# Kernel tuning notes

Hardware: AMD Instinct MI355X
Metric: run time of the kernel (lower is better)

The kernel has to match this reference:

```python
import jax, jax.numpy as jnp
import numpy as np

L_ORDER = 1
R_ORDER = 1
THRESHOLD = 1.0


def setup_inputs() -> dict:
    key = jax.random.key(0)
    k0, k1, k2, k3, k4 = jax.random.split(key, 5)
    B, T, D, K = 16, 2048, 512, L_ORDER + R_ORDER + 1
    hidden = jax.random.normal(k0, (B, T, D), jnp.float32)
    conv_w = jax.random.normal(k1, (D, 1, K), jnp.float32) / np.sqrt(K).astype(np.float32)
    conv_b = jax.random.normal(k2, (D,), jnp.float32) * 0.05
    lin_w = jax.random.normal(k3, (1, D), jnp.float32) / np.sqrt(D).astype(np.float32)
    lin_b = jax.random.normal(k4, (1,), jnp.float32) * 0.05
    return {"hidden": hidden, "conv_w": conv_w, "conv_b": conv_b, "lin_w": lin_w, "lin_b": lin_b}


def _alphas(hidden, conv_w, conv_b, lin_w, lin_b):
    # hidden: [B, T, D]
    ctx = jnp.transpose(hidden, (0, 2, 1))              # [B, D, T]
    q = jnp.pad(ctx, ((0, 0), (0, 0), (L_ORDER, R_ORDER)))
    mem = jax.lax.conv_general_dilated(
        q, conv_w, (1,), 'VALID',
        dimension_numbers=('NCH', 'OIH', 'NCH'),
        feature_group_count=ctx.shape[1]) + conv_b[None, :, None]   # depthwise conv
    out = jax.nn.relu(jnp.transpose(mem + ctx, (0, 2, 1)))          # [B, T, D] (dropout = identity in eval)
    logits = out @ lin_w.T + lin_b                                  # [B, T, 1]
    return jax.nn.sigmoid(logits)[..., 0]                           # [B, T]


def _cif_scan(hidden, alphas):
    # Sequential integrate-and-fire recurrence over time via lax.scan.
    B, T, H = hidden.shape

    def step(carry, xs):
        integ, frame = carry        # [B], [B, H]
        a, h = xs                   # [B], [B, H]
        dist = 1.0 - integ
        integ = integ + a
        fire_out = integ            # recorded pre-reset (matches torch list_fires)
        fire = integ >= THRESHOLD
        integ = jnp.where(fire, integ - 1.0, integ)
        cur = jnp.where(fire, dist, a)
        rem = a - cur
        frame_out = frame + cur[:, None] * h   # recorded pre-reset
        frame = jnp.where(fire[:, None], rem[:, None] * h, frame_out)
        return (integ, frame), (fire_out, frame_out)

    init = (jnp.zeros((B,), hidden.dtype), jnp.zeros((B, H), hidden.dtype))
    _, (fires, frames) = jax.lax.scan(
        step, init, (alphas.T, jnp.transpose(hidden, (1, 0, 2))))
    return jnp.transpose(fires, (1, 0)), jnp.transpose(frames, (1, 0, 2))  # [B,T], [B,T,H]


def reference(hidden, conv_w, conv_b, lin_w, lin_b):
    B, T, H = hidden.shape
    alphas = _alphas(hidden, conv_w, conv_b, lin_w, lin_b)   # [B, T]
    token_num = alphas.sum(-1)                               # [B]
    fires, frames = _cif_scan(hidden, alphas)
    # Ragged extraction: gather frames at fire positions, left-packed, zero-padded
    # to max_label_len = max(round(sum alphas)). Data-dependent length -> python int.
    max_label_len = int(jnp.max(jnp.round(token_num)))
    fire_mask = fires >= THRESHOLD                           # [B, T]
    rank = jnp.cumsum(fire_mask, axis=1) - 1                 # output slot per fire
    b_idx = jnp.arange(B)[:, None]
    vals = jnp.where(fire_mask[..., None], frames, 0.0)
    acoustic_embeds = jnp.zeros((B, max_label_len, H), hidden.dtype)
    acoustic_embeds = acoustic_embeds.at[b_idx, rank].add(vals, mode='drop')
    return acoustic_embeds, token_num, alphas, fires
```

## Files before the change

### kernel.cpp

```cpp
#include <hip/hip_runtime.h>
#include <math.h>

#define B_ 16
#define T_ 2048
#define D_ 512


__global__ __launch_bounds__(256) void k_alphas(
    const float* __restrict__ hidden,
    const float* __restrict__ conv_w,
    const float* __restrict__ conv_b,
    const float* __restrict__ lin_w,
    const float* __restrict__ lin_b,
    float* __restrict__ alphas_out)
{
    const int b    = blockIdx.y;
    const int wv   = threadIdx.x >> 6;
    const int lane = threadIdx.x & 63;
    const int t0   = blockIdx.x * 64 + wv * 16;
    const int d0   = lane * 8;

    float w0[8], w1[8], w2[8], cb[8], lw[8];
    #pragma unroll
    for (int i = 0; i < 8; ++i) {
        int d = d0 + i;
        w0[i] = conv_w[3 * d];
        w1[i] = conv_w[3 * d + 1];
        w2[i] = conv_w[3 * d + 2];
        cb[i] = conv_b[d];
        lw[i] = lin_w[d];
    }
    const float lb = lin_b[0];

    const float* rbase = hidden + (size_t)b * T_ * D_ + d0;
    auto loadrow = [&](int t, float* f) {
        const float4* p = (const float4*)(rbase + (size_t)t * D_);
        float4 x = p[0], y = p[1];
        f[0]=x.x; f[1]=x.y; f[2]=x.z; f[3]=x.w;
        f[4]=y.x; f[5]=y.y; f[6]=y.z; f[7]=y.w;
    };

    float hm[8], hc[8], hp[8], nx[8];
    if (t0 > 0) { loadrow(t0 - 1, hm); }
    else        { for (int i = 0; i < 8; ++i) hm[i] = 0.f; }
    loadrow(t0, hc);
    loadrow(t0 + 1, hp);

    float* aout = alphas_out + (size_t)b * T_;
    #pragma unroll 4
    for (int j = 0; j < 16; ++j) {
        const int t = t0 + j;
        const int tn = t + 2;
        if (tn < T_) { loadrow(tn, nx); }
        else         { for (int i = 0; i < 8; ++i) nx[i] = 0.f; }

        float dot = 0.f;
        #pragma unroll
        for (int i = 0; i < 8; ++i) {
            float mem = fmaf(hm[i], w0[i],
                        fmaf(hc[i], w1[i],
                        fmaf(hp[i], w2[i], cb[i])));
            float o = mem + hc[i];
            o = o > 0.f ? o : 0.f;
            dot += o * lw[i];
        }
        #pragma unroll
        for (int off = 32; off > 0; off >>= 1) dot += __shfl_down(dot, off);
        if (lane == 0) aout[t] = 1.f / (1.f + expf(-(dot + lb)));

        #pragma unroll
        for (int i = 0; i < 8; ++i) { hm[i] = hc[i]; hc[i] = hp[i]; hp[i] = nx[i]; }
    }
}

__global__ __launch_bounds__(256) void k_scan(
    const float* __restrict__ alphas_in,
    double* __restrict__ S,
    int*    __restrict__ fire_pos,
    int*    __restrict__ n_fires,
    float*  __restrict__ fires_out,
    float*  __restrict__ token_out)
{
    const int b = blockIdx.x, tid = threadIdx.x;
    const size_t base = (size_t)b * T_;

    double a[8], tsum = 0.0;
    #pragma unroll
    for (int i = 0; i < 8; ++i) { a[i] = (double)alphas_in[base + tid * 8 + i]; tsum += a[i]; }

    __shared__ double ssum[256];
    ssum[tid] = tsum;
    __syncthreads();
    for (int off = 1; off < 256; off <<= 1) {
        double v = (tid >= off) ? ssum[tid - off] : 0.0;
        __syncthreads();
        ssum[tid] += v;
        __syncthreads();
    }
    double run = ssum[tid] - tsum;

    #pragma unroll
    for (int i = 0; i < 8; ++i) {
        int t = tid * 8 + i;
        double Sp = run, fp = floor(Sp);
        run += a[i];
        S[base + t] = run;
        fires_out[base + t] = (float)(run - fp);
        if (run >= fp + 1.0) fire_pos[base + (long long)fp] = t;
    }
    if (tid == 255) {
        n_fires[b]   = (int)floor(run);
        token_out[b] = (float)run;
    }
}

__global__ __launch_bounds__(256) void k_gather(
    const float*  __restrict__ hidden,
    const double* __restrict__ S,
    const int*    __restrict__ fire_pos,
    const int*    __restrict__ n_fires,
    float* __restrict__ acoustic, int ML)
{
    const int s = blockIdx.x, b = blockIdx.y;
    float2* dst = (float2*)(acoustic + ((size_t)b * ML + s) * D_) + threadIdx.x;

    int nf = n_fires[b];
    if (nf > ML) nf = ML;
    if (s >= nf) { *dst = make_float2(0.f, 0.f); return; }

    const size_t base = (size_t)b * T_;
    const int t_end   = fire_pos[base + s];
    const int t_start = (s == 0) ? 0 : fire_pos[base + s - 1];

    const double vlo = (double)s, vhi = (double)(s + 1);
    float acc0 = 0.f, acc1 = 0.f;
    double Sp = (t_start == 0) ? 0.0 : S[base + t_start - 1];
    const float* hrow = hidden + (base + (size_t)t_start) * D_ + threadIdx.x * 2;
    for (int t = t_start; t <= t_end; ++t, hrow += D_) {
        double St = S[base + t];
        double wd = fmin(St, vhi) - fmax(Sp, vlo);
        float w = wd > 0.0 ? (float)wd : 0.f;
        float2 hv = *(const float2*)hrow;
        acc0 += w * hv.x;
        acc1 += w * hv.y;
        Sp = St;
    }
    *dst = make_float2(acc0, acc1);
}

extern "C" void kernel_launch(void* const* d_in, const int* in_sizes, int n_in,
                              void* d_out, int out_size, void* d_ws, size_t ws_size,
                              hipStream_t stream) {
    (void)in_sizes; (void)n_in; (void)ws_size;
    const float* hidden = (const float*)d_in[0];
    const float* conv_w = (const float*)d_in[1];
    const float* conv_b = (const float*)d_in[2];
    const float* lin_w  = (const float*)d_in[3];
    const float* lin_b  = (const float*)d_in[4];

    const int B = B_, T = T_, D = D_;
    int ML = (out_size - (B + 2 * B * T)) / (B * D);
    if (ML < 1) ML = 1;

    float* out        = (float*)d_out;
    float* acoustic   = out;
    float* token_out  = out + (size_t)B * ML * D;
    float* alphas_out = token_out + B;
    float* fires_out  = alphas_out + (size_t)B * T;

    double* S        = (double*)d_ws;
    int*    fire_pos = (int*)(S + (size_t)B * T);
    int*    n_fires  = fire_pos + (size_t)B * T;

    k_alphas<<<dim3(T / 64, B), 256, 0, stream>>>(hidden, conv_w, conv_b,
                                                  lin_w, lin_b, alphas_out);
    k_scan<<<B, 256, 0, stream>>>(alphas_out, S, fire_pos, n_fires,
                                  fires_out, token_out);
    k_gather<<<dim3(ML, B), 256, 0, stream>>>(hidden, S, fire_pos, n_fires,
                                              acoustic, ML);
}
```

Measured before the change: 132.0 us.

## Preload rows in alphas kernel, use wave-shuffle scan, widen gather loads

The alphas kernel now gives each wave 8 timesteps and loads all 10 needed rows into registers up front, so the loads are issued together instead of streamed one per step. The launch grid doubles to match. The scan replaces the shared-memory Hillis-Steele loop, which synchronised at every step, with a wave-level shuffle scan plus a small cross-wave fixup. The gather kernel uses float4 loads with 128 threads per block instead of float2 with 256. Together these aim to raise memory-level parallelism and cut barrier overhead, at the cost of more register use and more redundant halo loads in the alphas kernel.

```diff
diff --git a/kernel.cpp b/kernel.cpp
--- a/kernel.cpp
+++ b/kernel.cpp
@@ -17,7 +17,7 @@
     const int b    = blockIdx.y;
     const int wv   = threadIdx.x >> 6;
     const int lane = threadIdx.x & 63;
-    const int t0   = blockIdx.x * 64 + wv * 16;
+    const int t0   = blockIdx.x * 32 + wv * 8;
     const int d0   = lane * 8;
 
     float w0[8], w1[8], w2[8], cb[8], lw[8];
@@ -33,43 +33,38 @@
     const float lb = lin_b[0];
 
     const float* rbase = hidden + (size_t)b * T_ * D_ + d0;
-    auto loadrow = [&](int t, float* f) {
-        const float4* p = (const float4*)(rbase + (size_t)t * D_);
-        float4 x = p[0], y = p[1];
-        f[0]=x.x; f[1]=x.y; f[2]=x.z; f[3]=x.w;
-        f[4]=y.x; f[5]=y.y; f[6]=y.z; f[7]=y.w;
-    };
 
-    float hm[8], hc[8], hp[8], nx[8];
-    if (t0 > 0) { loadrow(t0 - 1, hm); }
-    else        { for (int i = 0; i < 8; ++i) hm[i] = 0.f; }
-    loadrow(t0, hc);
-    loadrow(t0 + 1, hp);
+    float r[10][8];
+    #pragma unroll
+    for (int k = 0; k < 10; ++k) {
+        const int t = t0 - 1 + k;
+        if (t >= 0 && t < T_) {
+            const float4* p = (const float4*)(rbase + (size_t)t * D_);
+            float4 x = p[0], y = p[1];
+            r[k][0]=x.x; r[k][1]=x.y; r[k][2]=x.z; r[k][3]=x.w;
+            r[k][4]=y.x; r[k][5]=y.y; r[k][6]=y.z; r[k][7]=y.w;
+        } else {
+            #pragma unroll
+            for (int i = 0; i < 8; ++i) r[k][i] = 0.f;
+        }
+    }
 
     float* aout = alphas_out + (size_t)b * T_;
-    #pragma unroll 4
-    for (int j = 0; j < 16; ++j) {
-        const int t = t0 + j;
-        const int tn = t + 2;
-        if (tn < T_) { loadrow(tn, nx); }
-        else         { for (int i = 0; i < 8; ++i) nx[i] = 0.f; }
-
+    #pragma unroll
+    for (int j = 0; j < 8; ++j) {
         float dot = 0.f;
         #pragma unroll
         for (int i = 0; i < 8; ++i) {
-            float mem = fmaf(hm[i], w0[i],
-                        fmaf(hc[i], w1[i],
-                        fmaf(hp[i], w2[i], cb[i])));
-            float o = mem + hc[i];
+            float mem = fmaf(r[j][i], w0[i],
+                        fmaf(r[j+1][i], w1[i],
+                        fmaf(r[j+2][i], w2[i], cb[i])));
+            float o = mem + r[j+1][i];
             o = o > 0.f ? o : 0.f;
             dot += o * lw[i];
         }
         #pragma unroll
         for (int off = 32; off > 0; off >>= 1) dot += __shfl_down(dot, off);
-        if (lane == 0) aout[t] = 1.f / (1.f + expf(-(dot + lb)));
-
-        #pragma unroll
-        for (int i = 0; i < 8; ++i) { hm[i] = hc[i]; hc[i] = hp[i]; hp[i] = nx[i]; }
+        if (lane == 0) aout[t0 + j] = 1.f / (1.f + expf(-(dot + lb)));
     }
 }
 
@@ -82,22 +77,32 @@
     float*  __restrict__ token_out)
 {
     const int b = blockIdx.x, tid = threadIdx.x;
+    const int wv = tid >> 6, lane = tid & 63;
     const size_t base = (size_t)b * T_;
 
-    double a[8], tsum = 0.0;
+    const float4* ap = (const float4*)(alphas_in + base + tid * 8);
+    float4 a0 = ap[0], a1 = ap[1];
+    double a[8];
+    a[0]=a0.x; a[1]=a0.y; a[2]=a0.z; a[3]=a0.w;
+    a[4]=a1.x; a[5]=a1.y; a[6]=a1.z; a[7]=a1.w;
+    double tsum = 0.0;
     #pragma unroll
-    for (int i = 0; i < 8; ++i) { a[i] = (double)alphas_in[base + tid * 8 + i]; tsum += a[i]; }
+    for (int i = 0; i < 8; ++i) tsum += a[i];
 
-    __shared__ double ssum[256];
-    ssum[tid] = tsum;
+    double incl = tsum;
+    #pragma unroll
+    for (int off = 1; off < 64; off <<= 1) {
+        double v = __shfl_up(incl, off);
+        if (lane >= off) incl += v;
+    }
+    __shared__ double wsum[4];
+    if (lane == 63) wsum[wv] = incl;
     __syncthreads();
-    for (int off = 1; off < 256; off <<= 1) {
-        double v = (tid >= off) ? ssum[tid - off] : 0.0;
-        __syncthreads();
-        ssum[tid] += v;
-        __syncthreads();
-    }
-    double run = ssum[tid] - tsum;
+    double wbase = 0.0;
+    #pragma unroll
+    for (int w = 0; w < 3; ++w) if (w < wv) wbase += wsum[w];
+
+    double run = wbase + incl - tsum;
 
     #pragma unroll
     for (int i = 0; i < 8; ++i) {
@@ -114,7 +119,7 @@
     }
 }
 
-__global__ __launch_bounds__(256) void k_gather(
+__global__ __launch_bounds__(128) void k_gather(
     const float*  __restrict__ hidden,
     const double* __restrict__ S,
     const int*    __restrict__ fire_pos,
@@ -122,30 +127,30 @@
     float* __restrict__ acoustic, int ML)
 {
     const int s = blockIdx.x, b = blockIdx.y;
-    float2* dst = (float2*)(acoustic + ((size_t)b * ML + s) * D_) + threadIdx.x;
+    float4* dst = (float4*)(acoustic + ((size_t)b * ML + s) * D_) + threadIdx.x;
 
     int nf = n_fires[b];
     if (nf > ML) nf = ML;
-    if (s >= nf) { *dst = make_float2(0.f, 0.f); return; }
+    if (s >= nf) { *dst = make_float4(0.f, 0.f, 0.f, 0.f); return; }
 
     const size_t base = (size_t)b * T_;
     const int t_end   = fire_pos[base + s];
     const int t_start = (s == 0) ? 0 : fire_pos[base + s - 1];
 
     const double vlo = (double)s, vhi = (double)(s + 1);
-    float acc0 = 0.f, acc1 = 0.f;
+    float a0 = 0.f, a1 = 0.f, a2 = 0.f, a3 = 0.f;
     double Sp = (t_start == 0) ? 0.0 : S[base + t_start - 1];
-    const float* hrow = hidden + (base + (size_t)t_start) * D_ + threadIdx.x * 2;
-    for (int t = t_start; t <= t_end; ++t, hrow += D_) {
+    const float4* hrow =
+        (const float4*)(hidden + (base + (size_t)t_start) * D_) + threadIdx.x;
+    for (int t = t_start; t <= t_end; ++t, hrow += D_ / 4) {
         double St = S[base + t];
         double wd = fmin(St, vhi) - fmax(Sp, vlo);
         float w = wd > 0.0 ? (float)wd : 0.f;
-        float2 hv = *(const float2*)hrow;
-        acc0 += w * hv.x;
-        acc1 += w * hv.y;
+        float4 hv = *hrow;
+        a0 += w * hv.x; a1 += w * hv.y; a2 += w * hv.z; a3 += w * hv.w;
         Sp = St;
     }
-    *dst = make_float2(acc0, acc1);
+    *dst = make_float4(a0, a1, a2, a3);
 }
 
 extern "C" void kernel_launch(void* const* d_in, const int* in_sizes, int n_in,
@@ -172,10 +177,10 @@
     int*    fire_pos = (int*)(S + (size_t)B * T);
     int*    n_fires  = fire_pos + (size_t)B * T;
 
-    k_alphas<<<dim3(T / 64, B), 256, 0, stream>>>(hidden, conv_w, conv_b,
+    k_alphas<<<dim3(T / 32, B), 256, 0, stream>>>(hidden, conv_w, conv_b,
                                                   lin_w, lin_b, alphas_out);
     k_scan<<<B, 256, 0, stream>>>(alphas_out, S, fire_pos, n_fires,
                                   fires_out, token_out);
-    k_gather<<<dim3(ML, B), 256, 0, stream>>>(hidden, S, fire_pos, n_fires,
+    k_gather<<<dim3(ML, B), 128, 0, stream>>>(hidden, S, fire_pos, n_fires,
                                               acoustic, ML);
 }
```

Measured after the change: 126.4 us (median of 2 runs). 4.2% less time.
